# Kernel tuning notes

Measured on AMD Instinct MI355X. Metric: run time of the kernel, lower is better.

## Reference

```python
import jax, jax.numpy as jnp
import numpy as np

N_NODES = 100000
N_EDGES = 1600000
D_IN = 128
D_HID = 128
D_OUT = 128


def setup_inputs() -> dict:
    key = jax.random.key(0)
    ks = jax.random.split(key, 8)
    x = jax.random.normal(ks[0], (N_NODES, D_IN), dtype=jnp.float32)
    src = jax.random.randint(ks[1], (N_EDGES,), 0, N_NODES, dtype=jnp.int32)
    dst = jax.random.randint(ks[2], (N_EDGES,), 0, N_NODES, dtype=jnp.int32)
    # GraphConv weight [D_IN, D_HID] and bias [D_HID] (DGL layout: h @ W)
    W = jax.random.normal(ks[3], (D_IN, D_HID), dtype=jnp.float32) / np.sqrt(D_IN)
    b = jnp.zeros((D_HID,), dtype=jnp.float32)
    # nn.Linear(hidden, output): weight [D_OUT, D_HID], bias [D_OUT]
    fc_W = jax.random.normal(ks[4], (D_OUT, D_HID), dtype=jnp.float32) / np.sqrt(D_HID)
    fc_b = jnp.zeros((D_OUT,), dtype=jnp.float32)
    return {"x": x, "src": src, "dst": dst, "W": W, "b": b, "fc_W": fc_W, "fc_b": fc_b}


def reference(x, src, dst, W, b, fc_W, fc_b):
    n = x.shape[0]
    ones = jnp.ones(src.shape[0], dtype=x.dtype)
    deg_out = jax.ops.segment_sum(ones, src, num_segments=n)  # out-degree of src nodes
    deg_in = jax.ops.segment_sum(ones, dst, num_segments=n)   # in-degree of dst nodes
    # DGL GraphConv norm='both': clamp degrees to min 1, use deg^{-1/2}
    norm_src = jax.lax.rsqrt(jnp.maximum(deg_out, 1.0))
    norm_dst = jax.lax.rsqrt(jnp.maximum(deg_in, 1.0))
    # message = (x * D_out^{-1/2})[src]; aggregate sum into dst
    msg = (x * norm_src[:, None])[src]                        # [E, D_IN]
    agg = jax.ops.segment_sum(msg, dst, num_segments=n)       # [N, D_IN]
    h = agg * norm_dst[:, None]
    h = h @ W + b                                             # GraphConv linear
    h = jax.nn.relu(h)
    out = h @ fc_W.T + fc_b                                   # nn.Linear
    return out
```

## Files before the change

kernel.cpp:

```cpp
#include <hip/hip_runtime.h>


#define BIN_SHIFT 9
#define BIN_RANGE 512

__global__ void zero_kernel(int* __restrict__ p, int n) {
  int i = blockIdx.x * blockDim.x + threadIdx.x;
  int stride = gridDim.x * blockDim.x;
  for (; i < n; i += stride) p[i] = 0;
}

__global__ void transpose128_kernel(const float* __restrict__ in, float* __restrict__ out) {
  int idx = blockIdx.x * 256 + threadIdx.x;
  int k = idx >> 7, j = idx & 127;
  out[idx] = in[j * 128 + k];
}

__global__ void deg_out_kernel(const int* __restrict__ src, int* __restrict__ deg_out, int E) {
  int i = blockIdx.x * blockDim.x + threadIdx.x;
  int e0 = i * 4;
  if (e0 + 3 < E) {
    int4 s4 = *(const int4*)&src[e0];
    atomicAdd(&deg_out[s4.x], 1);
    atomicAdd(&deg_out[s4.y], 1);
    atomicAdd(&deg_out[s4.z], 1);
    atomicAdd(&deg_out[s4.w], 1);
  } else {
    for (int e = e0; e < E; ++e) atomicAdd(&deg_out[src[e]], 1);
  }
}

__global__ __launch_bounds__(256) void bin_count_kernel(const int* __restrict__ dst,
                                                        int* __restrict__ binCnt, int E, int B) {
  __shared__ int h[256];
  int t = threadIdx.x;
  h[t] = 0;
  __syncthreads();
  int i = blockIdx.x * blockDim.x + t;
  int stride = gridDim.x * blockDim.x;
  for (; i < E; i += stride) atomicAdd(&h[dst[i] >> BIN_SHIFT], 1);
  __syncthreads();
  if (t < B && h[t]) atomicAdd(&binCnt[t], h[t]);
}

__global__ __launch_bounds__(256) void bin_scan_kernel(const int* __restrict__ binCnt,
                                                       int* __restrict__ binOff,
                                                       int* __restrict__ binCursor, int B) {
  __shared__ int s[256];
  int t = threadIdx.x;
  int v = (t < B) ? binCnt[t] : 0;
  s[t] = v;
  __syncthreads();
  for (int off = 1; off < 256; off <<= 1) {
    int a = (t >= off) ? s[t - off] : 0;
    __syncthreads();
    s[t] += a;
    __syncthreads();
  }
  int excl = s[t] - v;
  if (t < B) { binOff[t] = excl; binCursor[t] = excl; }
  if (t == B - 1) binOff[B] = excl + v;
}

__global__ __launch_bounds__(256) void bin_scatter_kernel(
    const int* __restrict__ src, const int* __restrict__ dst,
    int* __restrict__ binCursor, int* __restrict__ packed, int E, int B) {
  __shared__ int h[256];
  __shared__ int base[256];
  int t = threadIdx.x;
  int e0 = blockIdx.x * 4096;
  int eend = e0 + 4096 < E ? e0 + 4096 : E;
  h[t] = 0;
  __syncthreads();
  for (int e = e0 + t; e < eend; e += 256) atomicAdd(&h[dst[e] >> BIN_SHIFT], 1);
  __syncthreads();
  if (t < B) base[t] = h[t] ? atomicAdd(&binCursor[t], h[t]) : 0;
  __syncthreads();
  h[t] = 0;
  __syncthreads();
  for (int e = e0 + t; e < eend; e += 256) {
    int d = dst[e], s = src[e];
    int bin = d >> BIN_SHIFT;
    int p = atomicAdd(&h[bin], 1);
    packed[base[bin] + p] = s | ((d & (BIN_RANGE - 1)) << 17);
  }
}

__global__ __launch_bounds__(256) void bin_process_kernel(
    const int* __restrict__ packed, const int* __restrict__ binOff,
    int* __restrict__ csr_src, int* __restrict__ csr_off, int* __restrict__ deg_in, int N) {
  __shared__ int h[512];
  __shared__ int p2[256];
  int b = blockIdx.x, t = threadIdx.x;
  int lo = binOff[b], hi = binOff[b + 1];
  h[t] = 0; h[t + 256] = 0;
  __syncthreads();
  for (int i = lo + t; i < hi; i += 256) atomicAdd(&h[(packed[i] >> 17) & 511], 1);
  __syncthreads();
  int c0 = h[2 * t], c1 = h[2 * t + 1];
  int pair = c0 + c1;
  p2[t] = pair;
  __syncthreads();
  for (int off = 1; off < 256; off <<= 1) {
    int a = (t >= off) ? p2[t - off] : 0;
    __syncthreads();
    p2[t] += a;
    __syncthreads();
  }
  int epair = p2[t] - pair;
  int o0 = lo + epair, o1 = lo + epair + c0;
  int n0 = b * BIN_RANGE + 2 * t, n1 = n0 + 1;
  if (n0 < N) { csr_off[n0] = o0; deg_in[n0] = c0; }
  if (n1 < N) { csr_off[n1] = o1; deg_in[n1] = c1; }
  __syncthreads();
  h[2 * t] = o0;
  h[2 * t + 1] = o1;
  __syncthreads();
  for (int i = lo + t; i < hi; i += 256) {
    int pk = packed[i];
    int pos = atomicAdd(&h[(pk >> 17) & 511], 1);
    csr_src[pos] = pk & 0x1FFFF;
  }
}

__global__ void norm_kernel(const int* __restrict__ deg_out, const int* __restrict__ deg_in,
                            float* __restrict__ norm_src, float* __restrict__ norm_dst, int N) {
  int i = blockIdx.x * blockDim.x + threadIdx.x;
  if (i < N) {
    int dgo = deg_out[i]; if (dgo < 1) dgo = 1;
    int dgi = deg_in[i];  if (dgi < 1) dgi = 1;
    norm_src[i] = 1.0f / sqrtf((float)dgo);
    norm_dst[i] = 1.0f / sqrtf((float)dgi);
  }
}

__global__ __launch_bounds__(256) void agg_kernel(
    const float* __restrict__ x, const int* __restrict__ csr_src,
    const int* __restrict__ csr_off, const int* __restrict__ deg_in,
    const float* __restrict__ norm_src, const float* __restrict__ norm_dst,
    float* __restrict__ out, int N) {
  int wid = threadIdx.x >> 6;
  int lane = threadIdx.x & 63;
  int v = blockIdx.x * 4 + wid;
  if (v >= N) return;
  int start = csr_off[v];
  int cnt = deg_in[v];
  int end = start + cnt;
  const float2* __restrict__ x2 = (const float2*)x;

  float2 a0, a1, a2, a3;
  a0.x = a0.y = a1.x = a1.y = a2.x = a2.y = a3.x = a3.y = 0.f;

  int e = start;
  for (; e + 4 <= end; e += 4) {
    int s0 = csr_src[e + 0];
    int s1 = csr_src[e + 1];
    int s2 = csr_src[e + 2];
    int s3 = csr_src[e + 3];
    float n0 = norm_src[s0];
    float n1 = norm_src[s1];
    float n2 = norm_src[s2];
    float n3 = norm_src[s3];
    float2 v0 = x2[(size_t)s0 * 64 + lane];
    float2 v1 = x2[(size_t)s1 * 64 + lane];
    float2 v2 = x2[(size_t)s2 * 64 + lane];
    float2 v3 = x2[(size_t)s3 * 64 + lane];
    a0.x += v0.x * n0; a0.y += v0.y * n0;
    a1.x += v1.x * n1; a1.y += v1.y * n1;
    a2.x += v2.x * n2; a2.y += v2.y * n2;
    a3.x += v3.x * n3; a3.y += v3.y * n3;
  }
  for (; e < end; ++e) {
    int s = csr_src[e];
    float n = norm_src[s];
    float2 xv = x2[(size_t)s * 64 + lane];
    a0.x += xv.x * n; a0.y += xv.y * n;
  }

  float nd = norm_dst[v];
  float2 r;
  r.x = ((a0.x + a1.x) + (a2.x + a3.x)) * nd;
  r.y = ((a0.y + a1.y) + (a2.y + a3.y)) * nd;
  ((float2*)out)[(size_t)v * 64 + lane] = r;
}

__global__ __launch_bounds__(512) void gemm_fused_kernel(
    float* __restrict__ io, const float* __restrict__ W, const float* __restrict__ b,
    const float* __restrict__ fcwT, const float* __restrict__ fcb, int N) {
  __shared__ float aggT[64][132];
  __shared__ float hT[64][132];

  int t = threadIdx.x;
  int lane = t & 63;
  int wave = __builtin_amdgcn_readfirstlane(t >> 6);
  int j0 = wave * 16;
  int row0 = blockIdx.x * 64;
  size_t base = (size_t)row0 * 128;

  const float4* __restrict__ io4 = (const float4*)(io + base);
#pragma unroll
  for (int r = 0; r < 4; ++r) {
    int idx = r * 512 + t;
    int rr = idx >> 5;
    float4 v = make_float4(0.f, 0.f, 0.f, 0.f);
    if (row0 + rr < N) v = io4[idx];
    *(float4*)&aggT[rr][(idx & 31) * 4] = v;
  }
  __syncthreads();

  {
    float acc[16];
#pragma unroll
    for (int q = 0; q < 4; ++q) {
      float4 b4 = *(const float4*)&b[j0 + 4 * q];
      acc[4 * q + 0] = b4.x; acc[4 * q + 1] = b4.y;
      acc[4 * q + 2] = b4.z; acc[4 * q + 3] = b4.w;
    }
#pragma unroll 4
    for (int k4 = 0; k4 < 32; ++k4) {
      float4 a4 = *(const float4*)&aggT[lane][k4 * 4];
#pragma unroll
      for (int kk = 0; kk < 4; ++kk) {
        float av = (kk == 0) ? a4.x : (kk == 1) ? a4.y : (kk == 2) ? a4.z : a4.w;
        const float* Wrow = &W[(size_t)(k4 * 4 + kk) * 128 + j0];
#pragma unroll
        for (int q = 0; q < 4; ++q) {
          float4 w4 = *(const float4*)&Wrow[4 * q];
          acc[4 * q + 0] += av * w4.x;
          acc[4 * q + 1] += av * w4.y;
          acc[4 * q + 2] += av * w4.z;
          acc[4 * q + 3] += av * w4.w;
        }
      }
    }
#pragma unroll
    for (int q = 0; q < 4; ++q) {
      float4 h4;
      h4.x = fmaxf(acc[4 * q + 0], 0.f);
      h4.y = fmaxf(acc[4 * q + 1], 0.f);
      h4.z = fmaxf(acc[4 * q + 2], 0.f);
      h4.w = fmaxf(acc[4 * q + 3], 0.f);
      *(float4*)&hT[lane][j0 + 4 * q] = h4;
    }
  }
  __syncthreads();

  {
    float acc[16];
#pragma unroll
    for (int q = 0; q < 4; ++q) {
      float4 b4 = *(const float4*)&fcb[j0 + 4 * q];
      acc[4 * q + 0] = b4.x; acc[4 * q + 1] = b4.y;
      acc[4 * q + 2] = b4.z; acc[4 * q + 3] = b4.w;
    }
#pragma unroll 4
    for (int k4 = 0; k4 < 32; ++k4) {
      float4 a4 = *(const float4*)&hT[lane][k4 * 4];
#pragma unroll
      for (int kk = 0; kk < 4; ++kk) {
        float av = (kk == 0) ? a4.x : (kk == 1) ? a4.y : (kk == 2) ? a4.z : a4.w;
        const float* Wrow = &fcwT[(size_t)(k4 * 4 + kk) * 128 + j0];
#pragma unroll
        for (int q = 0; q < 4; ++q) {
          float4 w4 = *(const float4*)&Wrow[4 * q];
          acc[4 * q + 0] += av * w4.x;
          acc[4 * q + 1] += av * w4.y;
          acc[4 * q + 2] += av * w4.z;
          acc[4 * q + 3] += av * w4.w;
        }
      }
    }
#pragma unroll
    for (int q = 0; q < 4; ++q) {
      float4 o4;
      o4.x = acc[4 * q + 0]; o4.y = acc[4 * q + 1];
      o4.z = acc[4 * q + 2]; o4.w = acc[4 * q + 3];
      *(float4*)&aggT[lane][j0 + 4 * q] = o4;
    }
  }
  __syncthreads();

  float4* __restrict__ o4p = (float4*)(io + base);
#pragma unroll
  for (int r = 0; r < 4; ++r) {
    int idx = r * 512 + t;
    int rr = idx >> 5;
    if (row0 + rr < N) o4p[idx] = *(const float4*)&aggT[rr][(idx & 31) * 4];
  }
}

extern "C" void kernel_launch(void* const* d_in, const int* in_sizes, int n_in,
                              void* d_out, int out_size, void* d_ws, size_t ws_size,
                              hipStream_t stream) {
  const float* x   = (const float*)d_in[0];
  const int* src   = (const int*)d_in[1];
  const int* dst   = (const int*)d_in[2];
  const float* W   = (const float*)d_in[3];
  const float* b   = (const float*)d_in[4];
  const float* fcW = (const float*)d_in[5];
  const float* fcb = (const float*)d_in[6];
  float* out = (float*)d_out;

  const int N = in_sizes[0] / 128;
  const int E = in_sizes[1];
  const int B = (N + BIN_RANGE - 1) / BIN_RANGE;

  const int NA = ((N + 1023) / 1024) * 1024;
  int* wsi = (int*)d_ws;
  int*   deg_out_a = wsi + 0 * (size_t)NA;
  int*   binCnt    = wsi + 1 * (size_t)NA;
  int*   binOff    = binCnt + 256;
  int*   binCursor = binOff + 257;
  int*   deg_in    = wsi + 2 * (size_t)NA;
  int*   csr_off   = wsi + 3 * (size_t)NA;
  float* norm_src  = (float*)(wsi + 4 * (size_t)NA);
  float* norm_dst  = (float*)(wsi + 5 * (size_t)NA);
  float* fcwT      = (float*)(wsi + 6 * (size_t)NA);
  int*   packed    = wsi + 6 * (size_t)NA + 16384;
  int*   csr_src   = packed + E;

  zero_kernel<<<256, 256, 0, stream>>>(wsi, NA + 256);
  transpose128_kernel<<<64, 256, 0, stream>>>(fcW, fcwT);
  deg_out_kernel<<<(E / 4 + 255) / 256, 256, 0, stream>>>(src, deg_out_a, E);
  bin_count_kernel<<<512, 256, 0, stream>>>(dst, binCnt, E, B);
  bin_scan_kernel<<<1, 256, 0, stream>>>(binCnt, binOff, binCursor, B);
  bin_scatter_kernel<<<(E + 4095) / 4096, 256, 0, stream>>>(src, dst, binCursor, packed, E, B);
  bin_process_kernel<<<B, 256, 0, stream>>>(packed, binOff, csr_src, csr_off, deg_in, N);
  norm_kernel<<<(N + 255) / 256, 256, 0, stream>>>(deg_out_a, deg_in, norm_src, norm_dst, N);
  agg_kernel<<<(N + 3) / 4, 256, 0, stream>>>(x, csr_src, csr_off, deg_in,
                                              norm_src, norm_dst, out, N);
  gemm_fused_kernel<<<(N + 63) / 64, 512, 0, stream>>>(out, W, b, fcwT, fcb, N);
}
```

Baseline: 456.2 us.

## Prescale features to fp16 and compute out-degree via binned counting

Adds a prescale pass that multiplies x by norm_src once and stores it as half2, so the gather in aggregation reads half the bytes and no longer needs a per-edge norm_src lookup. The aggregation loop is unrolled to 8 edges with eight accumulators. The global-atomic out-degree kernel is replaced by a binned scatter and a per-bin shared-memory histogram, reusing the dst-binning approach. This adds extra passes over src and x and introduces fp16 rounding of the messages, which could affect accuracy.

```diff
diff --git a/kernel.cpp b/kernel.cpp
--- a/kernel.cpp
+++ b/kernel.cpp
@@ -1,4 +1,5 @@
 #include <hip/hip_runtime.h>
+#include <hip/hip_fp16.h>
 
 
 #define BIN_SHIFT 9
@@ -16,36 +17,31 @@
   out[idx] = in[j * 128 + k];
 }
 
-__global__ void deg_out_kernel(const int* __restrict__ src, int* __restrict__ deg_out, int E) {
-  int i = blockIdx.x * blockDim.x + threadIdx.x;
-  int e0 = i * 4;
-  if (e0 + 3 < E) {
-    int4 s4 = *(const int4*)&src[e0];
-    atomicAdd(&deg_out[s4.x], 1);
-    atomicAdd(&deg_out[s4.y], 1);
-    atomicAdd(&deg_out[s4.z], 1);
-    atomicAdd(&deg_out[s4.w], 1);
-  } else {
-    for (int e = e0; e < E; ++e) atomicAdd(&deg_out[src[e]], 1);
-  }
-}
-
-__global__ __launch_bounds__(256) void bin_count_kernel(const int* __restrict__ dst,
-                                                        int* __restrict__ binCnt, int E, int B) {
-  __shared__ int h[256];
+__global__ __launch_bounds__(256) void bin_count2_kernel(
+    const int* __restrict__ src, const int* __restrict__ dst,
+    int* __restrict__ binCnt, int* __restrict__ srcBinCnt, int E, int B) {
+  __shared__ int hd[256];
+  __shared__ int hs[256];
   int t = threadIdx.x;
-  h[t] = 0;
+  hd[t] = 0; hs[t] = 0;
   __syncthreads();
   int i = blockIdx.x * blockDim.x + t;
   int stride = gridDim.x * blockDim.x;
-  for (; i < E; i += stride) atomicAdd(&h[dst[i] >> BIN_SHIFT], 1);
-  __syncthreads();
-  if (t < B && h[t]) atomicAdd(&binCnt[t], h[t]);
-}
-
-__global__ __launch_bounds__(256) void bin_scan_kernel(const int* __restrict__ binCnt,
-                                                       int* __restrict__ binOff,
-                                                       int* __restrict__ binCursor, int B) {
+  for (; i < E; i += stride) {
+    atomicAdd(&hd[dst[i] >> BIN_SHIFT], 1);
+    atomicAdd(&hs[src[i] >> BIN_SHIFT], 1);
+  }
+  __syncthreads();
+  if (t < B) {
+    if (hd[t]) atomicAdd(&binCnt[t], hd[t]);
+    if (hs[t]) atomicAdd(&srcBinCnt[t], hs[t]);
+  }
+}
+
+__global__ __launch_bounds__(256) void bin_scan2_kernel(
+    const int* __restrict__ binCnt, int* __restrict__ binOff, int* __restrict__ binCursor,
+    const int* __restrict__ srcBinCnt, int* __restrict__ srcBinOff,
+    int* __restrict__ srcBinCursor, int B) {
   __shared__ int s[256];
   int t = threadIdx.x;
   int v = (t < B) ? binCnt[t] : 0;
@@ -60,6 +56,19 @@
   int excl = s[t] - v;
   if (t < B) { binOff[t] = excl; binCursor[t] = excl; }
   if (t == B - 1) binOff[B] = excl + v;
+  __syncthreads();
+  v = (t < B) ? srcBinCnt[t] : 0;
+  s[t] = v;
+  __syncthreads();
+  for (int off = 1; off < 256; off <<= 1) {
+    int a = (t >= off) ? s[t - off] : 0;
+    __syncthreads();
+    s[t] += a;
+    __syncthreads();
+  }
+  excl = s[t] - v;
+  if (t < B) { srcBinOff[t] = excl; srcBinCursor[t] = excl; }
+  if (t == B - 1) srcBinOff[B] = excl + v;
 }
 
 __global__ __launch_bounds__(256) void bin_scatter_kernel(
@@ -123,6 +132,45 @@
   }
 }
 
+__global__ __launch_bounds__(256) void bin_scatter_src_kernel(
+    const int* __restrict__ src, int* __restrict__ srcBinCursor,
+    int* __restrict__ packed, int E, int B) {
+  __shared__ int h[256];
+  __shared__ int base[256];
+  int t = threadIdx.x;
+  int e0 = blockIdx.x * 4096;
+  int eend = e0 + 4096 < E ? e0 + 4096 : E;
+  h[t] = 0;
+  __syncthreads();
+  for (int e = e0 + t; e < eend; e += 256) atomicAdd(&h[src[e] >> BIN_SHIFT], 1);
+  __syncthreads();
+  if (t < B) base[t] = h[t] ? atomicAdd(&srcBinCursor[t], h[t]) : 0;
+  __syncthreads();
+  h[t] = 0;
+  __syncthreads();
+  for (int e = e0 + t; e < eend; e += 256) {
+    int s = src[e];
+    int bin = s >> BIN_SHIFT;
+    int p = atomicAdd(&h[bin], 1);
+    packed[base[bin] + p] = s & (BIN_RANGE - 1);
+  }
+}
+
+__global__ __launch_bounds__(256) void bin_process_src_kernel(
+    const int* __restrict__ packed, const int* __restrict__ srcBinOff,
+    int* __restrict__ deg_out, int N) {
+  __shared__ int h[512];
+  int b = blockIdx.x, t = threadIdx.x;
+  int lo = srcBinOff[b], hi = srcBinOff[b + 1];
+  h[t] = 0; h[t + 256] = 0;
+  __syncthreads();
+  for (int i = lo + t; i < hi; i += 256) atomicAdd(&h[packed[i] & 511], 1);
+  __syncthreads();
+  int n0 = b * BIN_RANGE + t, n1 = n0 + 256;
+  if (n0 < N) deg_out[n0] = h[t];
+  if (n1 < N) deg_out[n1] = h[t + 256];
+}
+
 __global__ void norm_kernel(const int* __restrict__ deg_out, const int* __restrict__ deg_in,
                             float* __restrict__ norm_src, float* __restrict__ norm_dst, int N) {
   int i = blockIdx.x * blockDim.x + threadIdx.x;
@@ -134,11 +182,21 @@
   }
 }
 
+__global__ void prescale_kernel(const float2* __restrict__ x2, const float* __restrict__ ns,
+                                __half2* __restrict__ xs2, int n64) {
+  int i = blockIdx.x * blockDim.x + threadIdx.x;
+  int stride = gridDim.x * blockDim.x;
+  for (; i < n64; i += stride) {
+    float2 v = x2[i];
+    float nn = ns[i >> 6];
+    xs2[i] = __floats2half2_rn(v.x * nn, v.y * nn);
+  }
+}
+
 __global__ __launch_bounds__(256) void agg_kernel(
-    const float* __restrict__ x, const int* __restrict__ csr_src,
+    const __half2* __restrict__ xs2, const int* __restrict__ csr_src,
     const int* __restrict__ csr_off, const int* __restrict__ deg_in,
-    const float* __restrict__ norm_src, const float* __restrict__ norm_dst,
-    float* __restrict__ out, int N) {
+    const float* __restrict__ norm_dst, float* __restrict__ out, int N) {
   int wid = threadIdx.x >> 6;
   int lane = threadIdx.x & 63;
   int v = blockIdx.x * 4 + wid;
@@ -146,41 +204,63 @@
   int start = csr_off[v];
   int cnt = deg_in[v];
   int end = start + cnt;
-  const float2* __restrict__ x2 = (const float2*)x;
-
-  float2 a0, a1, a2, a3;
+
+  float2 a0, a1, a2, a3, a4, a5, a6, a7;
   a0.x = a0.y = a1.x = a1.y = a2.x = a2.y = a3.x = a3.y = 0.f;
+  a4.x = a4.y = a5.x = a5.y = a6.x = a6.y = a7.x = a7.y = 0.f;
 
   int e = start;
-  for (; e + 4 <= end; e += 4) {
+  for (; e + 8 <= end; e += 8) {
     int s0 = csr_src[e + 0];
     int s1 = csr_src[e + 1];
     int s2 = csr_src[e + 2];
     int s3 = csr_src[e + 3];
-    float n0 = norm_src[s0];
-    float n1 = norm_src[s1];
-    float n2 = norm_src[s2];
-    float n3 = norm_src[s3];
-    float2 v0 = x2[(size_t)s0 * 64 + lane];
-    float2 v1 = x2[(size_t)s1 * 64 + lane];
-    float2 v2 = x2[(size_t)s2 * 64 + lane];
-    float2 v3 = x2[(size_t)s3 * 64 + lane];
-    a0.x += v0.x * n0; a0.y += v0.y * n0;
-    a1.x += v1.x * n1; a1.y += v1.y * n1;
-    a2.x += v2.x * n2; a2.y += v2.y * n2;
-    a3.x += v3.x * n3; a3.y += v3.y * n3;
+    int s4 = csr_src[e + 4];
+    int s5 = csr_src[e + 5];
+    int s6 = csr_src[e + 6];
+    int s7 = csr_src[e + 7];
+    float2 f0 = __half22float2(xs2[(size_t)s0 * 64 + lane]);
+    float2 f1 = __half22float2(xs2[(size_t)s1 * 64 + lane]);
+    float2 f2 = __half22float2(xs2[(size_t)s2 * 64 + lane]);
+    float2 f3 = __half22float2(xs2[(size_t)s3 * 64 + lane]);
+    float2 f4 = __half22float2(xs2[(size_t)s4 * 64 + lane]);
+    float2 f5 = __half22float2(xs2[(size_t)s5 * 64 + lane]);
+    float2 f6 = __half22float2(xs2[(size_t)s6 * 64 + lane]);
+    float2 f7 = __half22float2(xs2[(size_t)s7 * 64 + lane]);
+    a0.x += f0.x; a0.y += f0.y;
+    a1.x += f1.x; a1.y += f1.y;
+    a2.x += f2.x; a2.y += f2.y;
+    a3.x += f3.x; a3.y += f3.y;
+    a4.x += f4.x; a4.y += f4.y;
+    a5.x += f5.x; a5.y += f5.y;
+    a6.x += f6.x; a6.y += f6.y;
+    a7.x += f7.x; a7.y += f7.y;
+  }
+  if (e + 4 <= end) {
+    int s0 = csr_src[e + 0];
+    int s1 = csr_src[e + 1];
+    int s2 = csr_src[e + 2];
+    int s3 = csr_src[e + 3];
+    float2 f0 = __half22float2(xs2[(size_t)s0 * 64 + lane]);
+    float2 f1 = __half22float2(xs2[(size_t)s1 * 64 + lane]);
+    float2 f2 = __half22float2(xs2[(size_t)s2 * 64 + lane]);
+    float2 f3 = __half22float2(xs2[(size_t)s3 * 64 + lane]);
+    a0.x += f0.x; a0.y += f0.y;
+    a1.x += f1.x; a1.y += f1.y;
+    a2.x += f2.x; a2.y += f2.y;
+    a3.x += f3.x; a3.y += f3.y;
+    e += 4;
   }
   for (; e < end; ++e) {
     int s = csr_src[e];
-    float n = norm_src[s];
-    float2 xv = x2[(size_t)s * 64 + lane];
-    a0.x += xv.x * n; a0.y += xv.y * n;
+    float2 f = __half22float2(xs2[(size_t)s * 64 + lane]);
+    a0.x += f.x; a0.y += f.y;
   }
 
   float nd = norm_dst[v];
   float2 r;
-  r.x = ((a0.x + a1.x) + (a2.x + a3.x)) * nd;
-  r.y = ((a0.y + a1.y) + (a2.y + a3.y)) * nd;
+  r.x = (((a0.x + a1.x) + (a2.x + a3.x)) + ((a4.x + a5.x) + (a6.x + a7.x))) * nd;
+  r.y = (((a0.y + a1.y) + (a2.y + a3.y)) + ((a4.y + a5.y) + (a6.y + a7.y))) * nd;
   ((float2*)out)[(size_t)v * 64 + lane] = r;
 }
 
@@ -307,27 +387,34 @@
 
   const int NA = ((N + 1023) / 1024) * 1024;
   int* wsi = (int*)d_ws;
-  int*   deg_out_a = wsi + 0 * (size_t)NA;
-  int*   binCnt    = wsi + 1 * (size_t)NA;
-  int*   binOff    = binCnt + 256;
-  int*   binCursor = binOff + 257;
-  int*   deg_in    = wsi + 2 * (size_t)NA;
-  int*   csr_off   = wsi + 3 * (size_t)NA;
-  float* norm_src  = (float*)(wsi + 4 * (size_t)NA);
-  float* norm_dst  = (float*)(wsi + 5 * (size_t)NA);
-  float* fcwT      = (float*)(wsi + 6 * (size_t)NA);
-  int*   packed    = wsi + 6 * (size_t)NA + 16384;
-  int*   csr_src   = packed + E;
-
-  zero_kernel<<<256, 256, 0, stream>>>(wsi, NA + 256);
+  int*   deg_out_a   = wsi;
+  int*   binCnt      = wsi + NA;
+  int*   srcBinCnt   = binCnt + 256;
+  int*   binOff      = srcBinCnt + 256;
+  int*   srcBinOff   = binOff + 257;
+  int*   binCursor   = srcBinOff + 257;
+  int*   srcBinCursor= binCursor + 256;
+  int*   deg_in      = srcBinCursor + 256;
+  int*   csr_off     = deg_in + NA;
+  float* norm_src    = (float*)(csr_off + NA);
+  float* norm_dst    = norm_src + NA;
+  float* fcwT        = norm_dst + NA;
+  int*   packed      = (int*)(fcwT + 16384);
+  int*   csr_src     = packed + E;
+  __half2* xs2       = (__half2*)(csr_src + E);
+
+  zero_kernel<<<256, 256, 0, stream>>>(wsi, NA + 512);
   transpose128_kernel<<<64, 256, 0, stream>>>(fcW, fcwT);
-  deg_out_kernel<<<(E / 4 + 255) / 256, 256, 0, stream>>>(src, deg_out_a, E);
-  bin_count_kernel<<<512, 256, 0, stream>>>(dst, binCnt, E, B);
-  bin_scan_kernel<<<1, 256, 0, stream>>>(binCnt, binOff, binCursor, B);
+  bin_count2_kernel<<<512, 256, 0, stream>>>(src, dst, binCnt, srcBinCnt, E, B);
+  bin_scan2_kernel<<<1, 256, 0, stream>>>(binCnt, binOff, binCursor,
+                                          srcBinCnt, srcBinOff, srcBinCursor, B);
   bin_scatter_kernel<<<(E + 4095) / 4096, 256, 0, stream>>>(src, dst, binCursor, packed, E, B);
   bin_process_kernel<<<B, 256, 0, stream>>>(packed, binOff, csr_src, csr_off, deg_in, N);
+  bin_scatter_src_kernel<<<(E + 4095) / 4096, 256, 0, stream>>>(src, srcBinCursor, packed, E, B);
+  bin_process_src_kernel<<<B, 256, 0, stream>>>(packed, srcBinOff, deg_out_a, N);
   norm_kernel<<<(N + 255) / 256, 256, 0, stream>>>(deg_out_a, deg_in, norm_src, norm_dst, N);
-  agg_kernel<<<(N + 3) / 4, 256, 0, stream>>>(x, csr_src, csr_off, deg_in,
-                                              norm_src, norm_dst, out, N);
+  prescale_kernel<<<2048, 256, 0, stream>>>((const float2*)x, norm_src, xs2, N * 64);
+  agg_kernel<<<(N + 3) / 4, 256, 0, stream>>>(xs2, csr_src, csr_off, deg_in,
+                                              norm_dst, out, N);
   gemm_fused_kernel<<<(N + 63) / 64, 512, 0, stream>>>(out, W, b, fcwT, fcb, N);
 }
```

Result: faster. 399.1 us (-12.5%).
